# Performance work log

Hardware: AMD Instinct MI355X
Metric: run time of the kernel (lower is better)

## Reference

```python
import jax, jax.numpy as jnp
import numpy as np

N_NODES = 100000
N_EDGES = 1600000
IN_C = 16
OUT_C = 16
N_EATTR = 8


def setup_inputs() -> dict:
    key = jax.random.key(0)
    k1, k2, k3, k4 = jax.random.split(key, 4)
    x = jax.random.normal(k1, (N_NODES, IN_C), dtype=jnp.float32)
    edge_index = jax.random.randint(k2, (2, N_EDGES), 0, N_NODES, dtype=jnp.int64)
    edge_attr = jax.random.normal(k3, (N_EDGES, N_EATTR), dtype=jnp.float32)
    # learned params (original inits to ones/zeros; use small random for a non-degenerate baseline)
    weight_matrix = jax.random.normal(k4, (N_EATTR, OUT_C, IN_C), dtype=jnp.float32) * 0.1
    bias = jnp.zeros((OUT_C,), dtype=jnp.float32)
    return {
        "x": x,
        "edge_index": edge_index,
        "edge_attr": edge_attr,
        "weight_matrix": weight_matrix,
        "bias": bias,
        "num_nodes": N_NODES,
    }


def reference(x, edge_index, edge_attr, weight_matrix, bias, num_nodes):
    # message: per-edge weight W_e = edge_attr @ weight_matrix (-> [E, out, in]),
    # then msg_e = W_e @ x[src_e]. Fused in one einsum to avoid the [E,out,in] blow-up.
    src = edge_index[0]
    dst = edge_index[1]
    x_j = x[src]                                   # [E, in]
    msg = jnp.einsum('ea,aoi,ei->eo', edge_attr, weight_matrix, x_j)  # [E, out]
    # aggregate: scatter-add messages to destination nodes
    aggr = jax.ops.segment_sum(msg, dst, num_segments=num_nodes)      # [N, out]
    # update: bias + relu
    return jax.nn.relu(aggr + bias)
```

## Files before the change

### kernel.cpp

```cpp
#include <hip/hip_runtime.h>


#define IN_C 16
#define OUT_C 16
#define NA 8

typedef unsigned short u16;
typedef unsigned int u32;
typedef short v2s __attribute__((ext_vector_type(2)));

__device__ __forceinline__ float bfbits(u32 hi) {
    union { u32 u; float f; } c; c.u = hi; return c.f;
}
__device__ __forceinline__ u16 f2bf(float f) {
    union { float f; u32 u; } c; c.f = f;
    u32 u = c.u + (0x7fffu + ((c.u >> 16) & 1u));
    return (u16)(u >> 16);
}
__device__ __forceinline__ float dot4(float4 a, float4 b) {
    float s = a.x * b.x;
    s = fmaf(a.y, b.y, s); s = fmaf(a.z, b.z, s); s = fmaf(a.w, b.w, s);
    return s;
}
__device__ __forceinline__ float dot8y(uint4 yu, float4 a0, float4 a1) {
    float s = bfbits(yu.x << 16) * a0.x;
    s = fmaf(bfbits(yu.x & 0xffff0000u), a0.y, s);
    s = fmaf(bfbits(yu.y << 16),         a0.z, s);
    s = fmaf(bfbits(yu.y & 0xffff0000u), a0.w, s);
    s = fmaf(bfbits(yu.z << 16),         a1.x, s);
    s = fmaf(bfbits(yu.z & 0xffff0000u), a1.y, s);
    s = fmaf(bfbits(yu.w << 16),         a1.z, s);
    s = fmaf(bfbits(yu.w & 0xffff0000u), a1.w, s);
    return s;
}

__global__ void __launch_bounds__(256) k_stage1(
    const float* __restrict__ x, const float* __restrict__ W,
    const int* __restrict__ ei, long long n_edges,
    u16* __restrict__ y, float* __restrict__ out,
    int* __restrict__ flag, int n_nodes) {
    __shared__ int s_nz;
    if (blockIdx.x == 0) {
        if (threadIdx.x == 0) s_nz = 0;
        __syncthreads();
        long long step = (n_edges / 256) | 1;
        long long pos = 1 + 2 * (long long)threadIdx.x * step;
        if (pos < 2 * n_edges && ei[pos] != 0) atomicOr(&s_nz, 1);
        __syncthreads();
        if (threadIdx.x == 0) flag[0] = (s_nz == 0) ? 1 : 0;
    }
    __shared__ float4 Wl[OUT_C][33];
    for (int k = threadIdx.x; k < 512; k += 256) {
        int a = k >> 6, o = (k >> 2) & 15, q = k & 3;
        Wl[o][a * 4 + q] = reinterpret_cast<const float4*>(W)[k];
    }
    __syncthreads();
    int npairs = (n_nodes + 1) >> 1;
    int idx = blockIdx.x * 256 + threadIdx.x;
    if (idx >= npairs * OUT_C) return;
    int p = idx >> 4, o = idx & 15;
    int n0 = p * 2;
    bool has1 = (n0 + 1) < n_nodes;
    const float4* xp0 = reinterpret_cast<const float4*>(x + (size_t)n0 * IN_C);
    float4 X0[4] = {xp0[0], xp0[1], xp0[2], xp0[3]};
    float4 X1[4];
    if (has1) {
        const float4* xp1 = reinterpret_cast<const float4*>(x + (size_t)(n0 + 1) * IN_C);
        X1[0] = xp1[0]; X1[1] = xp1[1]; X1[2] = xp1[2]; X1[3] = xp1[3];
    }
    union { uint4 u; u16 h[8]; } pk0, pk1;
#pragma unroll
    for (int a = 0; a < NA; ++a) {
        float4 w0 = Wl[o][a * 4 + 0], w1 = Wl[o][a * 4 + 1];
        float4 w2 = Wl[o][a * 4 + 2], w3 = Wl[o][a * 4 + 3];
        float s0 = dot4(w0, X0[0]) + dot4(w1, X0[1]) + dot4(w2, X0[2]) + dot4(w3, X0[3]);
        pk0.h[a] = f2bf(s0);
        if (has1) {
            float s1 = dot4(w0, X1[0]) + dot4(w1, X1[1]) + dot4(w2, X1[2]) + dot4(w3, X1[3]);
            pk1.h[a] = f2bf(s1);
        }
    }
    reinterpret_cast<uint4*>(y + ((size_t)n0 * OUT_C + o) * NA)[0] = pk0.u;
    out[(size_t)n0 * OUT_C + o] = 0.f;
    if (has1) {
        reinterpret_cast<uint4*>(y + ((size_t)(n0 + 1) * OUT_C + o) * NA)[0] = pk1.u;
        out[(size_t)(n0 + 1) * OUT_C + o] = 0.f;
    }
}

__global__ void __launch_bounds__(256) k_stage2_pk(
    const int* __restrict__ ei, const float* __restrict__ ea,
    const u16* __restrict__ y, u16* __restrict__ bufA, u16* __restrict__ bufB,
    const int* __restrict__ flag, long long n_edges) {
    long long gid = (long long)blockIdx.x * 256 + threadIdx.x;
    if (gid >= n_edges * 8) return;
    long long e = gid >> 3;
    int q = (int)(gid & 7);
    int src, dst;
    if (flag[0]) { src = ei[2 * e]; dst = ei[2 * (n_edges + e)]; }
    else         { src = ei[e];     dst = ei[n_edges + e]; }

    const float4* ap = reinterpret_cast<const float4*>(ea + e * NA);
    float4 a0 = ap[0], a1 = ap[1];

    const uint4* yp = reinterpret_cast<const uint4*>(y + ((size_t)src * OUT_C + 2 * q) * NA);
    float s0 = dot8y(yp[0], a0, a1);
    float s1 = dot8y(yp[1], a0, a1);

    union { v2s v; u16 h[2]; } pk;
    pk.h[0] = f2bf(s0);
    pk.h[1] = f2bf(s1);
    u16* target = (e & 1) ? bufB : bufA;
    v2s* addr = reinterpret_cast<v2s*>(target + (size_t)dst * OUT_C + 2 * q);
    __builtin_amdgcn_global_atomic_fadd_v2bf16(addr, pk.v);
}

__global__ void __launch_bounds__(256) k_final_pk(
    const u16* __restrict__ bufA, const u16* __restrict__ bufB,
    const float* __restrict__ bias, float* __restrict__ out, int total8) {
    int idx = blockIdx.x * 256 + threadIdx.x;
    if (idx >= total8) return;
    uint4 ua = reinterpret_cast<const uint4*>(bufA)[idx];
    uint4 ub = reinterpret_cast<const uint4*>(bufB)[idx];
    int ob = (idx & 1) * 8;
    const float4 b0 = reinterpret_cast<const float4*>(bias + ob)[0];
    const float4 b1 = reinterpret_cast<const float4*>(bias + ob + 4)[0];
    float fa[8], fb[8];
    u32 au[4] = {ua.x, ua.y, ua.z, ua.w}, bu[4] = {ub.x, ub.y, ub.z, ub.w};
#pragma unroll
    for (int j = 0; j < 4; ++j) {
        fa[2 * j]     = bfbits(au[j] << 16);
        fa[2 * j + 1] = bfbits(au[j] & 0xffff0000u);
        fb[2 * j]     = bfbits(bu[j] << 16);
        fb[2 * j + 1] = bfbits(bu[j] & 0xffff0000u);
    }
    float bb[8] = {b0.x, b0.y, b0.z, b0.w, b1.x, b1.y, b1.z, b1.w};
    float4 o0, o1;
    o0.x = fmaxf(fa[0] + fb[0] + bb[0], 0.f);
    o0.y = fmaxf(fa[1] + fb[1] + bb[1], 0.f);
    o0.z = fmaxf(fa[2] + fb[2] + bb[2], 0.f);
    o0.w = fmaxf(fa[3] + fb[3] + bb[3], 0.f);
    o1.x = fmaxf(fa[4] + fb[4] + bb[4], 0.f);
    o1.y = fmaxf(fa[5] + fb[5] + bb[5], 0.f);
    o1.z = fmaxf(fa[6] + fb[6] + bb[6], 0.f);
    o1.w = fmaxf(fa[7] + fb[7] + bb[7], 0.f);
    float4* op = reinterpret_cast<float4*>(out) + (size_t)idx * 2;
    op[0] = o0;
    op[1] = o1;
}

__global__ void __launch_bounds__(256) k_stage2(
    const int* __restrict__ ei, const float* __restrict__ ea,
    const u16* __restrict__ y, float* __restrict__ out,
    const int* __restrict__ flag, long long n_edges) {
    long long idx = (long long)blockIdx.x * 256 + threadIdx.x;
    if (idx >= n_edges * OUT_C) return;
    long long e = idx >> 4;
    int o = (int)(idx & 15);
    int src, dst;
    if (flag[0]) { src = ei[2 * e]; dst = ei[2 * (n_edges + e)]; }
    else         { src = ei[e];     dst = ei[n_edges + e]; }
    const float4* ap = reinterpret_cast<const float4*>(ea + e * NA);
    float4 a0 = ap[0], a1 = ap[1];
    uint4 yu = reinterpret_cast<const uint4*>(y + ((size_t)src * OUT_C + o) * NA)[0];
    float s = dot8y(yu, a0, a1);
    unsafeAtomicAdd(out + (size_t)dst * OUT_C + o, s);
}

__global__ void __launch_bounds__(256) k_bias_relu(
    const float* __restrict__ bias, float* __restrict__ out, int total4) {
    int idx = blockIdx.x * 256 + threadIdx.x;
    if (idx >= total4) return;
    int j0 = (idx & 3) * 4;
    const float4 b = reinterpret_cast<const float4*>(bias + j0)[0];
    float4* op = reinterpret_cast<float4*>(out) + idx;
    float4 v = op[0];
    v.x = fmaxf(v.x + b.x, 0.f);
    v.y = fmaxf(v.y + b.y, 0.f);
    v.z = fmaxf(v.z + b.z, 0.f);
    v.w = fmaxf(v.w + b.w, 0.f);
    op[0] = v;
}

__global__ void __launch_bounds__(256) k_direct(
    const float* __restrict__ x, const int* __restrict__ ei,
    const float* __restrict__ ea, const float* __restrict__ W,
    float* __restrict__ out, long long n_edges) {
    __shared__ float Wl[OUT_C][129];
    for (int k = threadIdx.x; k < NA * OUT_C * IN_C; k += 256) {
        int a = k >> 8, o = (k >> 4) & 15, i = k & 15;
        Wl[o][a * IN_C + i] = W[k];
    }
    __syncthreads();
    long long idx = (long long)blockIdx.x * 256 + threadIdx.x;
    if (idx >= n_edges * OUT_C) return;
    long long e = idx >> 4;
    int o = (int)(idx & 15);
    int src = ei[2 * e], dst = ei[2 * (n_edges + e)];
    const float4* ap = reinterpret_cast<const float4*>(ea + e * NA);
    float4 a0 = ap[0], a1 = ap[1];
    float av[NA] = {a0.x, a0.y, a0.z, a0.w, a1.x, a1.y, a1.z, a1.w};
    const float4* xp = reinterpret_cast<const float4*>(x + (size_t)src * IN_C);
    float4 x0 = xp[0], x1 = xp[1], x2 = xp[2], x3 = xp[3];
    float xv[16] = {x0.x, x0.y, x0.z, x0.w, x1.x, x1.y, x1.z, x1.w,
                    x2.x, x2.y, x2.z, x2.w, x3.x, x3.y, x3.z, x3.w};
    float s = 0.f;
#pragma unroll
    for (int a = 0; a < NA; ++a) {
        float d = 0.f;
#pragma unroll
        for (int i = 0; i < IN_C; ++i) d = fmaf(Wl[o][a * IN_C + i], xv[i], d);
        s = fmaf(av[a], d, s);
    }
    unsafeAtomicAdd(out + (size_t)dst * OUT_C + o, s);
}

static inline size_t a256(size_t v) { return (v + 255) & ~(size_t)255; }

extern "C" void kernel_launch(void* const* d_in, const int* in_sizes, int n_in,
                              void* d_out, int out_size, void* d_ws, size_t ws_size,
                              hipStream_t stream) {
    const float* x    = (const float*)d_in[0];
    const int*   ei   = (const int*)d_in[1];
    const float* ea   = (const float*)d_in[2];
    const float* W    = (const float*)d_in[3];
    const float* bias = (const float*)d_in[4];
    float* out = (float*)d_out;

    int n_nodes = in_sizes[0] / IN_C;
    long long E = in_sizes[2] / NA;

    size_t o_flag = 0;
    size_t o_y    = 256;
    size_t y_bytes = (size_t)n_nodes * OUT_C * NA * sizeof(u16);
    size_t o_bufA = o_y + a256(y_bytes);
    size_t buf_bytes = (size_t)n_nodes * OUT_C * sizeof(u16);
    size_t o_bufB = o_bufA + a256(buf_bytes);
    size_t total_pk = o_bufB + a256(buf_bytes);

    int npairs = (n_nodes + 1) >> 1;
    int g1 = (npairs * OUT_C + 255) / 256;

    if (ws_size >= total_pk) {
        int* flag = (int*)d_ws;
        u16* y    = (u16*)((char*)d_ws + o_y);
        u16* bufA = (u16*)((char*)d_ws + o_bufA);
        u16* bufB = (u16*)((char*)d_ws + o_bufB);
        hipMemsetAsync((char*)d_ws + o_bufA, 0, a256(buf_bytes) + a256(buf_bytes), stream);
        k_stage1<<<g1, 256, 0, stream>>>(x, W, ei, E, y, out, flag, n_nodes);
        long long t2 = E * 8;
        k_stage2_pk<<<(int)((t2 + 255) / 256), 256, 0, stream>>>(ei, ea, y, bufA, bufB, flag, E);
        int t3 = (n_nodes * OUT_C) / 8;
        k_final_pk<<<(t3 + 255) / 256, 256, 0, stream>>>(bufA, bufB, bias, out, t3);
    } else if (ws_size >= 256 + y_bytes) {
        int* flag = (int*)d_ws;
        u16* y    = (u16*)((char*)d_ws + o_y);
        k_stage1<<<g1, 256, 0, stream>>>(x, W, ei, E, y, out, flag, n_nodes);
        long long tE = E * OUT_C;
        k_stage2<<<(int)((tE + 255) / 256), 256, 0, stream>>>(ei, ea, y, out, flag, E);
        int t4 = (n_nodes * OUT_C) / 4;
        k_bias_relu<<<(t4 + 255) / 256, 256, 0, stream>>>(bias, out, t4);
    } else {
        hipMemsetAsync(d_out, 0, (size_t)n_nodes * OUT_C * sizeof(float), stream);
        long long tE = E * OUT_C;
        k_direct<<<(int)((tE + 255) / 256), 256, 0, stream>>>(x, ei, ea, W, out, E);
        int t4 = (n_nodes * OUT_C) / 4;
        k_bias_relu<<<(t4 + 255) / 256, 256, 0, stream>>>(bias, out, t4);
    }
}
```

Baseline: 200.8 us.

## Fold buffer zeroing into stage1, process two edges per thread with nontemporal loads

The separate memset of the bf16 accumulation buffers is replaced by extra blocks in the stage1 launch, which removes one launch. Stage2 now handles two edges per thread (p and p+half), issuing both sets of gathers before the atomics to raise memory-level parallelism. Streaming reads of edge indices and edge attributes use nontemporal loads so they do not evict the gathered y table from cache. The trade-offs are higher register pressure and half as many threads.

```diff
diff --git a/kernel.cpp b/kernel.cpp
--- a/kernel.cpp
+++ b/kernel.cpp
@@ -8,6 +8,7 @@
 typedef unsigned short u16;
 typedef unsigned int u32;
 typedef short v2s __attribute__((ext_vector_type(2)));
+typedef float v4f __attribute__((ext_vector_type(4)));
 
 __device__ __forceinline__ float bfbits(u32 hi) {
     union { u32 u; float f; } c; c.u = hi; return c.f;
@@ -22,7 +23,7 @@
     s = fmaf(a.y, b.y, s); s = fmaf(a.z, b.z, s); s = fmaf(a.w, b.w, s);
     return s;
 }
-__device__ __forceinline__ float dot8y(uint4 yu, float4 a0, float4 a1) {
+__device__ __forceinline__ float dot8y(uint4 yu, v4f a0, v4f a1) {
     float s = bfbits(yu.x << 16) * a0.x;
     s = fmaf(bfbits(yu.x & 0xffff0000u), a0.y, s);
     s = fmaf(bfbits(yu.y << 16),         a0.z, s);
@@ -38,7 +39,13 @@
     const float* __restrict__ x, const float* __restrict__ W,
     const int* __restrict__ ei, long long n_edges,
     u16* __restrict__ y, float* __restrict__ out,
-    int* __restrict__ flag, int n_nodes) {
+    int* __restrict__ flag, int n_nodes,
+    int main_blocks, uint4* __restrict__ zbase, int zcnt) {
+    if ((int)blockIdx.x >= main_blocks) {
+        int zi = ((int)blockIdx.x - main_blocks) * 256 + (int)threadIdx.x;
+        if (zi < zcnt) { uint4 z; z.x = z.y = z.z = z.w = 0u; zbase[zi] = z; }
+        return;
+    }
     __shared__ int s_nz;
     if (blockIdx.x == 0) {
         if (threadIdx.x == 0) s_nz = 0;
@@ -92,27 +99,60 @@
     const int* __restrict__ ei, const float* __restrict__ ea,
     const u16* __restrict__ y, u16* __restrict__ bufA, u16* __restrict__ bufB,
     const int* __restrict__ flag, long long n_edges) {
+    long long half = (n_edges + 1) >> 1;
     long long gid = (long long)blockIdx.x * 256 + threadIdx.x;
-    if (gid >= n_edges * 8) return;
-    long long e = gid >> 3;
+    if (gid >= half * 8) return;
+    long long p = gid >> 3;
     int q = (int)(gid & 7);
-    int src, dst;
-    if (flag[0]) { src = ei[2 * e]; dst = ei[2 * (n_edges + e)]; }
-    else         { src = ei[e];     dst = ei[n_edges + e]; }
-
-    const float4* ap = reinterpret_cast<const float4*>(ea + e * NA);
-    float4 a0 = ap[0], a1 = ap[1];
-
-    const uint4* yp = reinterpret_cast<const uint4*>(y + ((size_t)src * OUT_C + 2 * q) * NA);
-    float s0 = dot8y(yp[0], a0, a1);
-    float s1 = dot8y(yp[1], a0, a1);
-
-    union { v2s v; u16 h[2]; } pk;
-    pk.h[0] = f2bf(s0);
-    pk.h[1] = f2bf(s1);
-    u16* target = (e & 1) ? bufB : bufA;
-    v2s* addr = reinterpret_cast<v2s*>(target + (size_t)dst * OUT_C + 2 * q);
-    __builtin_amdgcn_global_atomic_fadd_v2bf16(addr, pk.v);
+    long long e1 = p + half;
+    bool has1 = e1 < n_edges;
+    int s0, d0, s1 = 0, d1 = 0;
+    if (flag[0]) {
+        s0 = __builtin_nontemporal_load(ei + 2 * p);
+        d0 = __builtin_nontemporal_load(ei + 2 * (n_edges + p));
+        if (has1) {
+            s1 = __builtin_nontemporal_load(ei + 2 * e1);
+            d1 = __builtin_nontemporal_load(ei + 2 * (n_edges + e1));
+        }
+    } else {
+        s0 = __builtin_nontemporal_load(ei + p);
+        d0 = __builtin_nontemporal_load(ei + n_edges + p);
+        if (has1) {
+            s1 = __builtin_nontemporal_load(ei + e1);
+            d1 = __builtin_nontemporal_load(ei + n_edges + e1);
+        }
+    }
+
+    const v4f* ap0 = reinterpret_cast<const v4f*>(ea + p * NA);
+    v4f a00 = __builtin_nontemporal_load(ap0);
+    v4f a01 = __builtin_nontemporal_load(ap0 + 1);
+    const uint4* yp0 = reinterpret_cast<const uint4*>(y + ((size_t)s0 * OUT_C + 2 * q) * NA);
+    uint4 y00 = yp0[0], y01 = yp0[1];
+
+    v4f a10, a11; uint4 y10, y11;
+    if (has1) {
+        const v4f* ap1 = reinterpret_cast<const v4f*>(ea + e1 * NA);
+        a10 = __builtin_nontemporal_load(ap1);
+        a11 = __builtin_nontemporal_load(ap1 + 1);
+        const uint4* yp1 = reinterpret_cast<const uint4*>(y + ((size_t)s1 * OUT_C + 2 * q) * NA);
+        y10 = yp1[0]; y11 = yp1[1];
+    }
+
+    union { v2s v; u16 h[2]; } pk0;
+    pk0.h[0] = f2bf(dot8y(y00, a00, a01));
+    pk0.h[1] = f2bf(dot8y(y01, a00, a01));
+    u16* t0 = (p & 1) ? bufB : bufA;
+    __builtin_amdgcn_global_atomic_fadd_v2bf16(
+        reinterpret_cast<v2s*>(t0 + (size_t)d0 * OUT_C + 2 * q), pk0.v);
+
+    if (has1) {
+        union { v2s v; u16 h[2]; } pk1;
+        pk1.h[0] = f2bf(dot8y(y10, a10, a11));
+        pk1.h[1] = f2bf(dot8y(y11, a10, a11));
+        u16* t1 = (e1 & 1) ? bufB : bufA;
+        __builtin_amdgcn_global_atomic_fadd_v2bf16(
+            reinterpret_cast<v2s*>(t1 + (size_t)d1 * OUT_C + 2 * q), pk1.v);
+    }
 }
 
 __global__ void __launch_bounds__(256) k_final_pk(
@@ -161,7 +201,9 @@
     if (flag[0]) { src = ei[2 * e]; dst = ei[2 * (n_edges + e)]; }
     else         { src = ei[e];     dst = ei[n_edges + e]; }
     const float4* ap = reinterpret_cast<const float4*>(ea + e * NA);
-    float4 a0 = ap[0], a1 = ap[1];
+    float4 af0 = ap[0], af1 = ap[1];
+    v4f a0 = {af0.x, af0.y, af0.z, af0.w};
+    v4f a1 = {af1.x, af1.y, af1.z, af1.w};
     uint4 yu = reinterpret_cast<const uint4*>(y + ((size_t)src * OUT_C + o) * NA)[0];
     float s = dot8y(yu, a0, a1);
     unsafeAtomicAdd(out + (size_t)dst * OUT_C + o, s);
@@ -246,16 +288,21 @@
         u16* y    = (u16*)((char*)d_ws + o_y);
         u16* bufA = (u16*)((char*)d_ws + o_bufA);
         u16* bufB = (u16*)((char*)d_ws + o_bufB);
-        hipMemsetAsync((char*)d_ws + o_bufA, 0, a256(buf_bytes) + a256(buf_bytes), stream);
-        k_stage1<<<g1, 256, 0, stream>>>(x, W, ei, E, y, out, flag, n_nodes);
-        long long t2 = E * 8;
+        size_t zero_bytes = a256(buf_bytes) + a256(buf_bytes);
+        int zcnt = (int)(zero_bytes / 16);
+        int gz = (zcnt + 255) / 256;
+        k_stage1<<<g1 + gz, 256, 0, stream>>>(x, W, ei, E, y, out, flag, n_nodes,
+                                              g1, (uint4*)((char*)d_ws + o_bufA), zcnt);
+        long long half = (E + 1) >> 1;
+        long long t2 = half * 8;
         k_stage2_pk<<<(int)((t2 + 255) / 256), 256, 0, stream>>>(ei, ea, y, bufA, bufB, flag, E);
         int t3 = (n_nodes * OUT_C) / 8;
         k_final_pk<<<(t3 + 255) / 256, 256, 0, stream>>>(bufA, bufB, bias, out, t3);
     } else if (ws_size >= 256 + y_bytes) {
         int* flag = (int*)d_ws;
         u16* y    = (u16*)((char*)d_ws + o_y);
-        k_stage1<<<g1, 256, 0, stream>>>(x, W, ei, E, y, out, flag, n_nodes);
+        k_stage1<<<g1, 256, 0, stream>>>(x, W, ei, E, y, out, flag, n_nodes,
+                                         g1, (uint4*)nullptr, 0);
         long long tE = E * OUT_C;
         k_stage2<<<(int)((tE + 255) / 256), 256, 0, stream>>>(ei, ea, y, out, flag, E);
         int t4 = (n_nodes * OUT_C) / 4;
```

New measurement: 207.7 us. 3.4% more time.

## Quantize per-node projected table to uint8 with per-node scale, fuse zeroing

Applied to the files above, without the earlier changes.

Replaces the bf16 per-node projected table y (256 B/node) with an 8-bit offset-quantized table (128 B/node) plus one float scale per node. The scale comes from a per-node max reduction across 16 lanes via shuffles, and the offset is undone in the edge kernel using the sum of edge attributes. This halves the random gather traffic in the edge stage. It also folds the accumulator-buffer memset into extra blocks of the stage-1 kernel to drop a separate launch. The cost is much lower precision (8-bit quantization), which may threaten accuracy tolerance, plus extra integer-to-float conversion work per edge.

```diff
diff --git a/kernel.cpp b/kernel.cpp
--- a/kernel.cpp
+++ b/kernel.cpp
@@ -7,7 +7,9 @@
 
 typedef unsigned short u16;
 typedef unsigned int u32;
+typedef unsigned char u8;
 typedef short v2s __attribute__((ext_vector_type(2)));
+typedef float v4f __attribute__((ext_vector_type(4)));
 
 __device__ __forceinline__ float bfbits(u32 hi) {
     union { u32 u; float f; } c; c.u = hi; return c.f;
@@ -22,23 +24,39 @@
     s = fmaf(a.y, b.y, s); s = fmaf(a.z, b.z, s); s = fmaf(a.w, b.w, s);
     return s;
 }
-__device__ __forceinline__ float dot8y(uint4 yu, float4 a0, float4 a1) {
-    float s = bfbits(yu.x << 16) * a0.x;
-    s = fmaf(bfbits(yu.x & 0xffff0000u), a0.y, s);
-    s = fmaf(bfbits(yu.y << 16),         a0.z, s);
-    s = fmaf(bfbits(yu.y & 0xffff0000u), a0.w, s);
-    s = fmaf(bfbits(yu.z << 16),         a1.x, s);
-    s = fmaf(bfbits(yu.z & 0xffff0000u), a1.y, s);
-    s = fmaf(bfbits(yu.w << 16),         a1.z, s);
-    s = fmaf(bfbits(yu.w & 0xffff0000u), a1.w, s);
+__device__ __forceinline__ float dotu8(u32 w0, u32 w1, v4f a0, v4f a1) {
+    float s = (float)(w0 & 255u) * a0.x;
+    s = fmaf((float)((w0 >> 8) & 255u),  a0.y, s);
+    s = fmaf((float)((w0 >> 16) & 255u), a0.z, s);
+    s = fmaf((float)(w0 >> 24),          a0.w, s);
+    s = fmaf((float)(w1 & 255u),         a1.x, s);
+    s = fmaf((float)((w1 >> 8) & 255u),  a1.y, s);
+    s = fmaf((float)((w1 >> 16) & 255u), a1.z, s);
+    s = fmaf((float)(w1 >> 24),          a1.w, s);
     return s;
+}
+__device__ __forceinline__ u32 pack4(const float* v, float r) {
+    u32 w = 0;
+#pragma unroll
+    for (int k = 0; k < 4; ++k) {
+        int q = (int)rintf(v[k] * r) + 128;
+        q = q < 0 ? 0 : (q > 255 ? 255 : q);
+        w |= ((u32)q) << (8 * k);
+    }
+    return w;
 }
 
 __global__ void __launch_bounds__(256) k_stage1(
     const float* __restrict__ x, const float* __restrict__ W,
     const int* __restrict__ ei, long long n_edges,
-    u16* __restrict__ y, float* __restrict__ out,
-    int* __restrict__ flag, int n_nodes) {
+    u8* __restrict__ y8, float* __restrict__ stab, float* __restrict__ out,
+    int* __restrict__ flag, int n_nodes,
+    int main_blocks, uint4* __restrict__ zbase, int zcnt) {
+    if ((int)blockIdx.x >= main_blocks) {
+        int zi = ((int)blockIdx.x - main_blocks) * 256 + (int)threadIdx.x;
+        if (zi < zcnt) { uint4 z; z.x = z.y = z.z = z.w = 0u; zbase[zi] = z; }
+        return;
+    }
     __shared__ int s_nz;
     if (blockIdx.x == 0) {
         if (threadIdx.x == 0) s_nz = 0;
@@ -68,29 +86,44 @@
         const float4* xp1 = reinterpret_cast<const float4*>(x + (size_t)(n0 + 1) * IN_C);
         X1[0] = xp1[0]; X1[1] = xp1[1]; X1[2] = xp1[2]; X1[3] = xp1[3];
     }
-    union { uint4 u; u16 h[8]; } pk0, pk1;
+    float v0[NA], v1[NA];
 #pragma unroll
     for (int a = 0; a < NA; ++a) {
         float4 w0 = Wl[o][a * 4 + 0], w1 = Wl[o][a * 4 + 1];
         float4 w2 = Wl[o][a * 4 + 2], w3 = Wl[o][a * 4 + 3];
-        float s0 = dot4(w0, X0[0]) + dot4(w1, X0[1]) + dot4(w2, X0[2]) + dot4(w3, X0[3]);
-        pk0.h[a] = f2bf(s0);
-        if (has1) {
-            float s1 = dot4(w0, X1[0]) + dot4(w1, X1[1]) + dot4(w2, X1[2]) + dot4(w3, X1[3]);
-            pk1.h[a] = f2bf(s1);
-        }
-    }
-    reinterpret_cast<uint4*>(y + ((size_t)n0 * OUT_C + o) * NA)[0] = pk0.u;
+        v0[a] = dot4(w0, X0[0]) + dot4(w1, X0[1]) + dot4(w2, X0[2]) + dot4(w3, X0[3]);
+        v1[a] = has1 ? (dot4(w0, X1[0]) + dot4(w1, X1[1]) + dot4(w2, X1[2]) + dot4(w3, X1[3]))
+                     : 0.f;
+    }
+    float m0 = 0.f, m1 = 0.f;
+#pragma unroll
+    for (int a = 0; a < NA; ++a) {
+        m0 = fmaxf(m0, fabsf(v0[a]));
+        m1 = fmaxf(m1, fabsf(v1[a]));
+    }
+#pragma unroll
+    for (int w = 1; w < 16; w <<= 1) {
+        m0 = fmaxf(m0, __shfl_xor(m0, w));
+        m1 = fmaxf(m1, __shfl_xor(m1, w));
+    }
+    float r0 = m0 > 0.f ? 127.f / m0 : 0.f;
+    float r1 = m1 > 0.f ? 127.f / m1 : 0.f;
+    uint2 q0; q0.x = pack4(v0, r0); q0.y = pack4(v0 + 4, r0);
+    reinterpret_cast<uint2*>(y8 + (size_t)n0 * 128 + o * 8)[0] = q0;
     out[(size_t)n0 * OUT_C + o] = 0.f;
+    if (o == 0) stab[n0] = m0 * (1.f / 127.f);
     if (has1) {
-        reinterpret_cast<uint4*>(y + ((size_t)(n0 + 1) * OUT_C + o) * NA)[0] = pk1.u;
+        uint2 q1; q1.x = pack4(v1, r1); q1.y = pack4(v1 + 4, r1);
+        reinterpret_cast<uint2*>(y8 + (size_t)(n0 + 1) * 128 + o * 8)[0] = q1;
         out[(size_t)(n0 + 1) * OUT_C + o] = 0.f;
+        if (o == 0) stab[n0 + 1] = m1 * (1.f / 127.f);
     }
 }
 
 __global__ void __launch_bounds__(256) k_stage2_pk(
     const int* __restrict__ ei, const float* __restrict__ ea,
-    const u16* __restrict__ y, u16* __restrict__ bufA, u16* __restrict__ bufB,
+    const u8* __restrict__ y8, const float* __restrict__ stab,
+    u16* __restrict__ bufA, u16* __restrict__ bufB,
     const int* __restrict__ flag, long long n_edges) {
     long long gid = (long long)blockIdx.x * 256 + threadIdx.x;
     if (gid >= n_edges * 8) return;
@@ -100,12 +133,15 @@
     if (flag[0]) { src = ei[2 * e]; dst = ei[2 * (n_edges + e)]; }
     else         { src = ei[e];     dst = ei[n_edges + e]; }
 
-    const float4* ap = reinterpret_cast<const float4*>(ea + e * NA);
-    float4 a0 = ap[0], a1 = ap[1];
-
-    const uint4* yp = reinterpret_cast<const uint4*>(y + ((size_t)src * OUT_C + 2 * q) * NA);
-    float s0 = dot8y(yp[0], a0, a1);
-    float s1 = dot8y(yp[1], a0, a1);
+    const v4f* ap = reinterpret_cast<const v4f*>(ea + e * NA);
+    v4f a0 = ap[0], a1 = ap[1];
+    float sumea = ((a0.x + a0.y) + (a0.z + a0.w)) + ((a1.x + a1.y) + (a1.z + a1.w));
+    float s = stab[src];
+
+    uint4 yq = reinterpret_cast<const uint4*>(y8 + (size_t)src * 128 + q * 16)[0];
+    float fix = -128.f * sumea;
+    float s0 = s * (dotu8(yq.x, yq.y, a0, a1) + fix);
+    float s1 = s * (dotu8(yq.z, yq.w, a0, a1) + fix);
 
     union { v2s v; u16 h[2]; } pk;
     pk.h[0] = f2bf(s0);
@@ -151,8 +187,8 @@
 
 __global__ void __launch_bounds__(256) k_stage2(
     const int* __restrict__ ei, const float* __restrict__ ea,
-    const u16* __restrict__ y, float* __restrict__ out,
-    const int* __restrict__ flag, long long n_edges) {
+    const u8* __restrict__ y8, const float* __restrict__ stab,
+    float* __restrict__ out, const int* __restrict__ flag, long long n_edges) {
     long long idx = (long long)blockIdx.x * 256 + threadIdx.x;
     if (idx >= n_edges * OUT_C) return;
     long long e = idx >> 4;
@@ -160,10 +196,12 @@
     int src, dst;
     if (flag[0]) { src = ei[2 * e]; dst = ei[2 * (n_edges + e)]; }
     else         { src = ei[e];     dst = ei[n_edges + e]; }
-    const float4* ap = reinterpret_cast<const float4*>(ea + e * NA);
-    float4 a0 = ap[0], a1 = ap[1];
-    uint4 yu = reinterpret_cast<const uint4*>(y + ((size_t)src * OUT_C + o) * NA)[0];
-    float s = dot8y(yu, a0, a1);
+    const v4f* ap = reinterpret_cast<const v4f*>(ea + e * NA);
+    v4f a0 = ap[0], a1 = ap[1];
+    float sumea = ((a0.x + a0.y) + (a0.z + a0.w)) + ((a1.x + a1.y) + (a1.z + a1.w));
+    float sc = stab[src];
+    uint2 yq = reinterpret_cast<const uint2*>(y8 + (size_t)src * 128 + o * 8)[0];
+    float s = sc * (dotu8(yq.x, yq.y, a0, a1) - 128.f * sumea);
     unsafeAtomicAdd(out + (size_t)dst * OUT_C + o, s);
 }
 
@@ -230,9 +268,10 @@
     int n_nodes = in_sizes[0] / IN_C;
     long long E = in_sizes[2] / NA;
 
-    size_t o_flag = 0;
-    size_t o_y    = 256;
-    size_t y_bytes = (size_t)n_nodes * OUT_C * NA * sizeof(u16);
+    size_t o_stab = 256;
+    size_t stab_bytes = (size_t)n_nodes * sizeof(float);
+    size_t o_y    = o_stab + a256(stab_bytes);
+    size_t y_bytes = (size_t)n_nodes * 128;
     size_t o_bufA = o_y + a256(y_bytes);
     size_t buf_bytes = (size_t)n_nodes * OUT_C * sizeof(u16);
     size_t o_bufB = o_bufA + a256(buf_bytes);
@@ -242,22 +281,29 @@
     int g1 = (npairs * OUT_C + 255) / 256;
 
     if (ws_size >= total_pk) {
-        int* flag = (int*)d_ws;
-        u16* y    = (u16*)((char*)d_ws + o_y);
+        int* flag  = (int*)d_ws;
+        float* stab = (float*)((char*)d_ws + o_stab);
+        u8*  y8   = (u8*)((char*)d_ws + o_y);
         u16* bufA = (u16*)((char*)d_ws + o_bufA);
         u16* bufB = (u16*)((char*)d_ws + o_bufB);
-        hipMemsetAsync((char*)d_ws + o_bufA, 0, a256(buf_bytes) + a256(buf_bytes), stream);
-        k_stage1<<<g1, 256, 0, stream>>>(x, W, ei, E, y, out, flag, n_nodes);
+        size_t zero_bytes = a256(buf_bytes) + a256(buf_bytes);
+        int zcnt = (int)(zero_bytes / 16);
+        int gz = (zcnt + 255) / 256;
+        k_stage1<<<g1 + gz, 256, 0, stream>>>(x, W, ei, E, y8, stab, out, flag, n_nodes,
+                                              g1, (uint4*)((char*)d_ws + o_bufA), zcnt);
         long long t2 = E * 8;
-        k_stage2_pk<<<(int)((t2 + 255) / 256), 256, 0, stream>>>(ei, ea, y, bufA, bufB, flag, E);
+        k_stage2_pk<<<(int)((t2 + 255) / 256), 256, 0, stream>>>(ei, ea, y8, stab,
+                                                                 bufA, bufB, flag, E);
         int t3 = (n_nodes * OUT_C) / 8;
         k_final_pk<<<(t3 + 255) / 256, 256, 0, stream>>>(bufA, bufB, bias, out, t3);
-    } else if (ws_size >= 256 + y_bytes) {
-        int* flag = (int*)d_ws;
-        u16* y    = (u16*)((char*)d_ws + o_y);
-        k_stage1<<<g1, 256, 0, stream>>>(x, W, ei, E, y, out, flag, n_nodes);
+    } else if (ws_size >= o_y + y_bytes) {
+        int* flag  = (int*)d_ws;
+        float* stab = (float*)((char*)d_ws + o_stab);
+        u8*  y8   = (u8*)((char*)d_ws + o_y);
+        k_stage1<<<g1, 256, 0, stream>>>(x, W, ei, E, y8, stab, out, flag, n_nodes,
+                                         g1, (uint4*)nullptr, 0);
         long long tE = E * OUT_C;
-        k_stage2<<<(int)((tE + 255) / 256), 256, 0, stream>>>(ei, ea, y, out, flag, E);
+        k_stage2<<<(int)((tE + 255) / 256), 256, 0, stream>>>(ei, ea, y8, stab, out, flag, E);
         int t4 = (n_nodes * OUT_C) / 4;
         k_bias_relu<<<(t4 + 255) / 256, 256, 0, stream>>>(bias, out, t4);
     } else {
```

Measured after the change: 198.9 us. About the same (-1.0%).
